# Kernel tuning notes

Measured on AMD Instinct MI355X. Metric: run time of the kernel, lower is better.

The kernel has to match this reference:

```python
import jax, jax.numpy as jnp
import numpy as np

B, D, T = 32, 256, 2048
Z_NUM, Z_DIM = 1024, 256


def setup_inputs() -> dict:
    key = jax.random.key(0)
    k1, k2 = jax.random.split(key)
    z = jax.random.normal(k1, (B, D, T), dtype=jnp.float32)
    embedding = jax.random.normal(k2, (Z_NUM, Z_DIM), dtype=jnp.float32)
    return {"z": z, "embedding": embedding}


def reference(z, embedding):
    # z: [B, D, T] (time_last=True), embedding: [z_num, z_dim]
    Bv, Dv, Tv = z.shape
    sg = jax.lax.stop_gradient
    # flatten to [N, D] with N = B*T
    zf = jnp.transpose(z, (0, 2, 1)).reshape(-1, Dv)
    # squared-euclidean distances [N, z_num]
    distances = (jnp.sum(zf * zf, axis=1, keepdims=True)
                 + jnp.sum(embedding * embedding, axis=1)
                 - 2.0 * (zf @ embedding.T))
    encoding_idx = jnp.argmin(distances, axis=1)          # [N]
    z_vq = embedding[encoding_idx]                        # [N, D] codebook gather
    # perplexity via scatter-add histogram (equiv. to one-hot scatter + column sum)
    counts = jnp.zeros((embedding.shape[0],), zf.dtype).at[encoding_idx].add(1.0)
    avg_probs = counts / zf.shape[0]
    perplexity = jnp.exp(-jnp.sum(avg_probs * jnp.log(avg_probs + 1e-10)))
    # commitment / codebook losses (reduction='mean', normalize=False)
    z_qut_loss = jnp.mean((z_vq - sg(zf)) ** 2)
    z_enc_loss = jnp.mean((sg(z_vq) - zf) ** 2)
    # straight-through estimator
    z_vq_st = zf + sg(z_vq - zf)
    out = jnp.transpose(z_vq_st.reshape(Bv, Tv, Dv), (0, 2, 1))  # back to [B, D, T]
    return out, z_qut_loss, z_enc_loss, perplexity
```

## Files before the change

### kernel.cpp

```cpp
#include <hip/hip_runtime.h>


typedef _Float16 f16;
typedef _Float16 f16x8 __attribute__((ext_vector_type(8)));
typedef float f32x4 __attribute__((ext_vector_type(4)));

#define NROWS 65536
#define THRESH 0.02f
#define AMB_CAP 32768

#define MERGE_T2(v1, i1, v2, i2, ov1, oi1, ov2, oi2)                      \
  do {                                                                    \
    if (ov1 < v1 || (ov1 == v1 && oi1 < i1)) {                            \
      if (v1 < ov2 || (v1 == ov2 && i1 < oi2)) { v2 = v1; i2 = i1; }      \
      else { v2 = ov2; i2 = oi2; }                                        \
      v1 = ov1; i1 = oi1;                                                 \
    } else if (ov1 < v2 || (ov1 == v2 && oi1 < i2)) { v2 = ov1; i2 = oi1; } \
  } while (0)

__device__ __forceinline__ void gl16(const void* g, void* l) {
  __builtin_amdgcn_global_load_lds(
      (const __attribute__((address_space(1))) unsigned int*)g,
      (__attribute__((address_space(3))) unsigned int*)l, 16, 0, 0);
}

__global__ void k0_prep(const float* __restrict__ emb, f16* __restrict__ eh,
                        f16* __restrict__ el, float* __restrict__ enorm,
                        float* __restrict__ counts, float* __restrict__ loss,
                        int* __restrict__ ambc) {
  int c = blockIdx.x, d = threadIdx.x;
  float v = emb[c * 256 + d];
  f16 h = (f16)v;
  f16 l = (f16)(v - (float)h);
  int chunk = c >> 7, crow = c & 127;
  int ks = d >> 5, gg = (d >> 3) & 3, e = d & 7;
  size_t off = ((((size_t)chunk * 8 + ks) * 4 + gg) * 128 + crow) * 8 + e;
  eh[off] = h;
  el[off] = l;
  float s = v * v;
#pragma unroll
  for (int o = 32; o; o >>= 1) s += __shfl_down(s, o, 64);
  __shared__ float red[4];
  if ((d & 63) == 0) red[d >> 6] = s;
  __syncthreads();
  if (d == 0) enorm[c] = red[0] + red[1] + red[2] + red[3];
  if (c == 0) {
    for (int i = d; i < 1024; i += 256) counts[i] = 0.f;
    if (d == 0) { *loss = 0.f; *ambc = 0; }
  }
}

__global__ void kp_split(const float* __restrict__ z, f16* __restrict__ zh,
                         f16* __restrict__ zl) {
  __shared__ float F[64][65];
  int bid = blockIdx.x;
  int b = bid >> 7;
  int rem = bid & 127;
  int t0 = (rem >> 2) << 6;
  int dd0 = (rem & 3) << 6;
  int tid = threadIdx.x;
  int tl = tid & 63, dr = tid >> 6;
  const float* zp = z + ((size_t)b * 256 + dd0 + dr) * 2048 + t0 + tl;
#pragma unroll
  for (int i = 0; i < 16; ++i)
    F[dr + i * 4][tl] = zp[(size_t)i * 4 * 2048];
  __syncthreads();
  int r = tid >> 2, q = tid & 3;
  f16x8 h0, h1, l0, l1;
#pragma unroll
  for (int j = 0; j < 8; ++j) {
    float v = F[q * 16 + j][r];
    f16 h = (f16)v; h0[j] = h; l0[j] = (f16)(v - (float)h);
  }
#pragma unroll
  for (int j = 0; j < 8; ++j) {
    float v = F[q * 16 + 8 + j][r];
    f16 h = (f16)v; h1[j] = h; l1[j] = (f16)(v - (float)h);
  }
  int n = b * 2048 + t0 + r;
  int rt = n >> 7, row = n & 127;
  int d0 = dd0 + q * 16;
  int ks = d0 >> 5, g0 = (d0 >> 3) & 3;
  size_t base = ((((size_t)rt * 8 + ks) * 4 + g0) * 128 + row) * 8;
  *(f16x8*)(zh + base) = h0; *(f16x8*)(zh + base + 1024) = h1;
  *(f16x8*)(zl + base) = l0; *(f16x8*)(zl + base + 1024) = l1;
}

__launch_bounds__(256, 3)
__global__ void k1p_argmin(const f16* __restrict__ zh, const f16* __restrict__ zl,
                           const f16* __restrict__ eh, const f16* __restrict__ el,
                           const float* __restrict__ enorm,
                           float* __restrict__ cv1, int* __restrict__ ci1,
                           float* __restrict__ cv2, int* __restrict__ ci2) {
  __shared__ f16x8 Ah[512], Al[512], Bh[512], Bl[512];
  __shared__ float en_s[128];
  __shared__ float rv1[256], rv2[256];
  __shared__ int ri1[256], ri2[256];

  int bid = blockIdx.x;
  int x = bid & 7, j = bid >> 3;
  int rowTile = x * 64 + (j >> 3);
  int chunk = j & 7;
  int cBase = chunk << 7;

  int tid = threadIdx.x;
  int lane = tid & 63;
  int w = tid >> 6;
  int wr = w >> 1, wc = w & 1;
  int g = lane >> 4, r16 = lane & 15;

  if (tid < 128) en_s[tid] = enorm[cBase + tid];

  f32x4 acc[4][4] = {};

  const char* gAh = (const char*)zh + (size_t)rowTile * 65536 + w * 2048 + lane * 16;
  const char* gAl = (const char*)zl + (size_t)rowTile * 65536 + w * 2048 + lane * 16;
  const char* gBh = (const char*)eh + (size_t)chunk * 65536 + w * 2048 + lane * 16;
  const char* gBl = (const char*)el + (size_t)chunk * 65536 + w * 2048 + lane * 16;
  char* lAh = (char*)Ah + w * 2048;
  char* lAl = (char*)Al + w * 2048;
  char* lBh = (char*)Bh + w * 2048;
  char* lBl = (char*)Bl + w * 2048;

  for (int ks = 0; ks < 8; ++ks) {
    if (ks) __syncthreads();
    size_t go = (size_t)ks * 8192;
    gl16(gAh + go, lAh);  gl16(gAh + go + 1024, lAh + 1024);
    gl16(gAl + go, lAl);  gl16(gAl + go + 1024, lAl + 1024);
    gl16(gBh + go, lBh);  gl16(gBh + go + 1024, lBh + 1024);
    gl16(gBl + go, lBl);  gl16(gBl + go + 1024, lBl + 1024);
    __syncthreads();
    f16x8 bh[4], bl[4];
#pragma unroll
    for (int ni = 0; ni < 4; ++ni) {
      int code = wc * 64 + ni * 16 + r16;
      bh[ni] = Bh[g * 128 + code];
      bl[ni] = Bl[g * 128 + code];
    }
#pragma unroll
    for (int mi = 0; mi < 4; ++mi) {
      int row = wr * 64 + mi * 16 + r16;
      f16x8 ah = Ah[g * 128 + row];
      f16x8 al = Al[g * 128 + row];
#pragma unroll
      for (int ni = 0; ni < 4; ++ni) {
        acc[mi][ni] = __builtin_amdgcn_mfma_f32_16x16x32_f16(ah, bh[ni], acc[mi][ni], 0, 0, 0);
        acc[mi][ni] = __builtin_amdgcn_mfma_f32_16x16x32_f16(ah, bl[ni], acc[mi][ni], 0, 0, 0);
        acc[mi][ni] = __builtin_amdgcn_mfma_f32_16x16x32_f16(al, bh[ni], acc[mi][ni], 0, 0, 0);
      }
    }
  }
  float en[4];
#pragma unroll
  for (int ni = 0; ni < 4; ++ni) en[ni] = en_s[wc * 64 + ni * 16 + r16];
#pragma unroll
  for (int mi = 0; mi < 4; ++mi) {
#pragma unroll
    for (int r = 0; r < 4; ++r) {
      float v1 = 1e38f, v2 = 1e38f; int i1 = 0x7fffffff, i2 = 0x7fffffff;
#pragma unroll
      for (int ni = 0; ni < 4; ++ni) {
        float v = en[ni] - 2.0f * acc[mi][ni][r];
        int idx = cBase + wc * 64 + ni * 16 + r16;
        if (v < v1 || (v == v1 && idx < i1)) { v2 = v1; i2 = i1; v1 = v; i1 = idx; }
        else if (v < v2 || (v == v2 && idx < i2)) { v2 = v; i2 = idx; }
      }
#pragma unroll
      for (int o = 1; o < 16; o <<= 1) {
        float ov1 = __shfl_xor(v1, o, 64); int oi1 = __shfl_xor(i1, o, 64);
        float ov2 = __shfl_xor(v2, o, 64); int oi2 = __shfl_xor(i2, o, 64);
        MERGE_T2(v1, i1, v2, i2, ov1, oi1, ov2, oi2);
      }
      if (r16 == 0) {
        int row = wr * 64 + mi * 16 + g * 4 + r;
        rv1[row * 2 + wc] = v1; ri1[row * 2 + wc] = i1;
        rv2[row * 2 + wc] = v2; ri2[row * 2 + wc] = i2;
      }
    }
  }
  __syncthreads();
  if (tid < 128) {
    float v1 = rv1[tid * 2], ov1 = rv1[tid * 2 + 1];
    int   i1 = ri1[tid * 2], oi1 = ri1[tid * 2 + 1];
    float v2 = rv2[tid * 2], ov2 = rv2[tid * 2 + 1];
    int   i2 = ri2[tid * 2], oi2 = ri2[tid * 2 + 1];
    MERGE_T2(v1, i1, v2, i2, ov1, oi1, ov2, oi2);
    size_t n = (size_t)rowTile * 128 + tid;
    cv1[(size_t)chunk * NROWS + n] = v1;
    ci1[(size_t)chunk * NROWS + n] = i1;
    cv2[(size_t)chunk * NROWS + n] = v2;
    ci2[(size_t)chunk * NROWS + n] = i2;
  }
}

__global__ void k2_select(const float* __restrict__ cv1, const int* __restrict__ ci1,
                          const float* __restrict__ cv2, const int* __restrict__ ci2,
                          int* __restrict__ fidx, int* __restrict__ ambc,
                          int* __restrict__ amb_list) {
  int n = blockIdx.x * 256 + threadIdx.x;
  float g1 = 1e38f, g2 = 1e38f; int gi1 = 0x7fffffff, gi2 = 0x7fffffff;
#pragma unroll
  for (int c = 0; c < 8; ++c) {
    float ov1 = cv1[c * NROWS + n]; int oi1 = ci1[c * NROWS + n];
    float ov2 = cv2[c * NROWS + n]; int oi2 = ci2[c * NROWS + n];
    MERGE_T2(g1, gi1, g2, gi2, ov1, oi1, ov2, oi2);
  }
  fidx[n] = gi1;
  if (g2 - g1 < THRESH) {
    int pos = atomicAdd(ambc, 1);
    if (pos < AMB_CAP) amb_list[pos] = n;
  }
}

__global__ void k2b_rescore(const float* __restrict__ z, const float* __restrict__ emb,
                            const float* __restrict__ enorm,
                            const int* __restrict__ ci1, const int* __restrict__ ci2,
                            const int* __restrict__ ambc, const int* __restrict__ amb_list,
                            int* __restrict__ fidx) {
  int cnt = *ambc; if (cnt > AMB_CAP) cnt = AMB_CAP;
  int lane = threadIdx.x & 63;
  int wglobal = (blockIdx.x * 256 + threadIdx.x) >> 6;
  for (int a = wglobal; a < cnt; a += 256) {
    int n = amb_list[a];
    int bb = n >> 11, t = n & 2047;
    float zr[4];
#pragma unroll
    for (int jj = 0; jj < 4; ++jj)
      zr[jj] = z[((size_t)bb * 256 + lane * 4 + jj) * 2048 + t];
    float zn = zr[0] * zr[0] + zr[1] * zr[1] + zr[2] * zr[2] + zr[3] * zr[3];
#pragma unroll
    for (int o = 1; o < 64; o <<= 1) zn += __shfl_xor(zn, o, 64);
    float bv = 1e38f; int bi = 0x7fffffff;
    for (int cc = 0; cc < 16; ++cc) {
      int c = cc >> 1;
      int cand = (cc & 1) ? ci2[c * NROWS + n] : ci1[c * NROWS + n];
      const float4* e4p = (const float4*)(emb + (size_t)cand * 256);
      float4 e4 = e4p[lane];
      float s = zr[0] * e4.x + zr[1] * e4.y + zr[2] * e4.z + zr[3] * e4.w;
#pragma unroll
      for (int o = 1; o < 64; o <<= 1) s += __shfl_xor(s, o, 64);
      float d = zn + enorm[cand] - 2.0f * s;
      if (d < bv || (d == bv && cand < bi)) { bv = d; bi = cand; }
    }
    if (lane == 0) fidx[n] = bi;
  }
}

__global__ void k3_gather(const float* __restrict__ z, const float* __restrict__ emb,
                          const int* __restrict__ fidx, float* __restrict__ out,
                          float* __restrict__ counts, float* __restrict__ loss) {
  __shared__ int sidx[128];
  __shared__ float red[4];
  int rowTile = blockIdx.x;
  int bb = rowTile >> 4;
  int t0 = (rowTile & 15) << 7;
  int tid = threadIdx.x;
  if (tid < 128) sidx[tid] = fidx[rowTile * 128 + tid];
  __syncthreads();
  int q = tid & 31, dh = (tid >> 5) << 5;
  const float* e0 = emb + (size_t)sidx[q * 4 + 0] * 256;
  const float* e1 = emb + (size_t)sidx[q * 4 + 1] * 256;
  const float* e2 = emb + (size_t)sidx[q * 4 + 2] * 256;
  const float* e3 = emb + (size_t)sidx[q * 4 + 3] * 256;
  size_t zb = ((size_t)bb * 256 + dh) * 2048 + t0 + q * 4;
  float ls = 0.f;
  for (int i = 0; i < 32; ++i) {
    int d = dh + i;
    float4 z4 = *(const float4*)(z + zb + (size_t)i * 2048);
    float4 e4 = make_float4(e0[d], e1[d], e2[d], e3[d]);
    *(float4*)(out + zb + (size_t)i * 2048) = e4;
    float da = e4.x - z4.x, db = e4.y - z4.y, dc = e4.z - z4.z, dd = e4.w - z4.w;
    ls += da * da + db * db + dc * dc + dd * dd;
  }
#pragma unroll
  for (int o = 32; o; o >>= 1) ls += __shfl_down(ls, o, 64);
  if ((tid & 63) == 0) red[tid >> 6] = ls;
  __syncthreads();
  if (tid == 0) atomicAdd(loss, red[0] + red[1] + red[2] + red[3]);
  if (tid < 128) atomicAdd(counts + sidx[tid], 1.0f);
}

__global__ void k4_final(const float* __restrict__ counts, const float* __restrict__ loss,
                         float* __restrict__ outs) {
  __shared__ float red[4];
  int tid = threadIdx.x;
  float h = 0.f;
  for (int i = tid; i < 1024; i += 256) {
    float p = counts[i] * (1.0f / 65536.0f);
    h += p * logf(p + 1e-10f);
  }
#pragma unroll
  for (int o = 32; o; o >>= 1) h += __shfl_down(h, o, 64);
  if ((tid & 63) == 0) red[tid >> 6] = h;
  __syncthreads();
  if (tid == 0) {
    float H = red[0] + red[1] + red[2] + red[3];
    float perp = expf(-H);
    float l = *loss * (1.0f / 16777216.0f);
    outs[0] = l;
    outs[1] = l;
    outs[2] = perp;
  }
}

extern "C" void kernel_launch(void* const* d_in, const int* in_sizes, int n_in,
                              void* d_out, int out_size, void* d_ws, size_t ws_size,
                              hipStream_t stream) {
  const float* z = (const float*)d_in[0];
  const float* emb = (const float*)d_in[1];
  float* out = (float*)d_out;
  char* ws = (char*)d_ws;
  f16*   eh     = (f16*)(ws);
  f16*   el     = (f16*)(ws + (512u << 10));
  float* enorm  = (float*)(ws + (1u << 20));
  float* counts = (float*)(ws + (1u << 20) + 4096);
  float* lossp  = (float*)(ws + (1u << 20) + 8192);
  int*   ambc   = (int*)  (ws + (1u << 20) + 8196);
  int*   amb_l  = (int*)  (ws + (1u << 20) + 16384);
  float* cv1    = (float*)(ws + (2u << 20));
  int*   ci1    = (int*)  (ws + (4u << 20));
  float* cv2    = (float*)(ws + (6u << 20));
  int*   ci2    = (int*)  (ws + (8u << 20));
  int*   fidx   = (int*)  (ws + (10u << 20));
  f16*   zh     = (f16*)(ws + (11u << 20));
  f16*   zl     = (f16*)(ws + (43u << 20));

  hipLaunchKernelGGL(k0_prep,     dim3(1024), dim3(256), 0, stream, emb, eh, el, enorm, counts, lossp, ambc);
  hipLaunchKernelGGL(kp_split,    dim3(4096), dim3(256), 0, stream, z, zh, zl);
  hipLaunchKernelGGL(k1p_argmin,  dim3(4096), dim3(256), 0, stream, zh, zl, eh, el, enorm, cv1, ci1, cv2, ci2);
  hipLaunchKernelGGL(k2_select,   dim3(256), dim3(256), 0, stream, cv1, ci1, cv2, ci2, fidx, ambc, amb_l);
  hipLaunchKernelGGL(k2b_rescore, dim3(64),  dim3(256), 0, stream, z, emb, enorm, ci1, ci2, ambc, amb_l, fidx);
  hipLaunchKernelGGL(k3_gather,   dim3(512), dim3(256), 0, stream, z, emb, fidx, out, counts, lossp);
  hipLaunchKernelGGL(k4_final,    dim3(1),   dim3(256), 0, stream, counts, lossp, out + 16777216);
}
```

Measured before the change: 360.3 us.

## Double-buffer LDS tiles in argmin GEMM to overlap loads with MFMA

Adds a second LDS buffer for the A/B hi/lo tiles in the distance-GEMM argmin kernel. The next k-step is prefetched with global_load_lds while MFMAs run on the current buffer, and there is one barrier per iteration instead of two. The aim is to hide global-load latency behind compute. In exchange, LDS use per block doubles and launch bounds drop from 3 to 2 blocks per CU, which cuts occupancy.

```diff
diff --git a/kernel.cpp b/kernel.cpp
--- a/kernel.cpp
+++ b/kernel.cpp
@@ -86,13 +86,13 @@
   *(f16x8*)(zl + base) = l0; *(f16x8*)(zl + base + 1024) = l1;
 }
 
-__launch_bounds__(256, 3)
+__launch_bounds__(256, 2)
 __global__ void k1p_argmin(const f16* __restrict__ zh, const f16* __restrict__ zl,
                            const f16* __restrict__ eh, const f16* __restrict__ el,
                            const float* __restrict__ enorm,
                            float* __restrict__ cv1, int* __restrict__ ci1,
                            float* __restrict__ cv2, int* __restrict__ ci2) {
-  __shared__ f16x8 Ah[512], Al[512], Bh[512], Bl[512];
+  __shared__ f16x8 Ah[2][512], Al[2][512], Bh[2][512], Bl[2][512];
   __shared__ float en_s[128];
   __shared__ float rv1[256], rv2[256];
   __shared__ int ri1[256], ri2[256];
@@ -117,31 +117,38 @@
   const char* gAl = (const char*)zl + (size_t)rowTile * 65536 + w * 2048 + lane * 16;
   const char* gBh = (const char*)eh + (size_t)chunk * 65536 + w * 2048 + lane * 16;
   const char* gBl = (const char*)el + (size_t)chunk * 65536 + w * 2048 + lane * 16;
-  char* lAh = (char*)Ah + w * 2048;
-  char* lAl = (char*)Al + w * 2048;
-  char* lBh = (char*)Bh + w * 2048;
-  char* lBl = (char*)Bl + w * 2048;
-
+
+  auto STAGE = [&](int b, int ks) {
+    size_t go = (size_t)ks * 8192;
+    char* dAh = (char*)&Ah[b][0] + w * 2048;
+    char* dAl = (char*)&Al[b][0] + w * 2048;
+    char* dBh = (char*)&Bh[b][0] + w * 2048;
+    char* dBl = (char*)&Bl[b][0] + w * 2048;
+    gl16(gAh + go, dAh);  gl16(gAh + go + 1024, dAh + 1024);
+    gl16(gAl + go, dAl);  gl16(gAl + go + 1024, dAl + 1024);
+    gl16(gBh + go, dBh);  gl16(gBh + go + 1024, dBh + 1024);
+    gl16(gBl + go, dBl);  gl16(gBl + go + 1024, dBl + 1024);
+  };
+
+  STAGE(0, 0);
+  __syncthreads();
+
+#pragma unroll
   for (int ks = 0; ks < 8; ++ks) {
-    if (ks) __syncthreads();
-    size_t go = (size_t)ks * 8192;
-    gl16(gAh + go, lAh);  gl16(gAh + go + 1024, lAh + 1024);
-    gl16(gAl + go, lAl);  gl16(gAl + go + 1024, lAl + 1024);
-    gl16(gBh + go, lBh);  gl16(gBh + go + 1024, lBh + 1024);
-    gl16(gBl + go, lBl);  gl16(gBl + go + 1024, lBl + 1024);
-    __syncthreads();
+    int cur = ks & 1;
+    if (ks < 7) STAGE(cur ^ 1, ks + 1);
     f16x8 bh[4], bl[4];
 #pragma unroll
     for (int ni = 0; ni < 4; ++ni) {
       int code = wc * 64 + ni * 16 + r16;
-      bh[ni] = Bh[g * 128 + code];
-      bl[ni] = Bl[g * 128 + code];
+      bh[ni] = Bh[cur][g * 128 + code];
+      bl[ni] = Bl[cur][g * 128 + code];
     }
 #pragma unroll
     for (int mi = 0; mi < 4; ++mi) {
       int row = wr * 64 + mi * 16 + r16;
-      f16x8 ah = Ah[g * 128 + row];
-      f16x8 al = Al[g * 128 + row];
+      f16x8 ah = Ah[cur][g * 128 + row];
+      f16x8 al = Al[cur][g * 128 + row];
 #pragma unroll
       for (int ni = 0; ni < 4; ++ni) {
         acc[mi][ni] = __builtin_amdgcn_mfma_f32_16x16x32_f16(ah, bh[ni], acc[mi][ni], 0, 0, 0);
@@ -149,6 +156,7 @@
         acc[mi][ni] = __builtin_amdgcn_mfma_f32_16x16x32_f16(al, bh[ni], acc[mi][ni], 0, 0, 0);
       }
     }
+    if (ks < 7) __syncthreads();
   }
   float en[4];
 #pragma unroll
```

Result: slower. 421.6 us (+17.0%).
